# Kernel optimization log

Hardware: AMD Instinct MI355X
Metric: run time of the kernel (lower is better)

The kernel has to match this reference:

```python
import jax, jax.numpy as jnp
import numpy as np

N_ATOMS = 100_000
N_PAIRS = 3_200_000


def setup_inputs() -> dict:
    key = jax.random.key(0)
    k0, k1, k2, k3, k4 = jax.random.split(key, 5)
    atomic_numbers = jax.random.randint(k0, (N_ATOMS,), 1, 95, dtype=jnp.int32)
    distances = jax.random.uniform(k1, (N_PAIRS,), jnp.float32, 0.5, 5.0)
    cutoffs = jax.random.uniform(k2, (N_PAIRS,), jnp.float32)
    idx_i = jnp.sort(jax.random.randint(k3, (N_PAIRS,), 0, N_ATOMS, dtype=jnp.int32))
    idx_j = jax.random.randint(k4, (N_PAIRS,), 0, N_ATOMS, dtype=jnp.int32)
    # ZBL parameters (trainable=True defaults from __init__)
    a_coefficient = jnp.array([0.8854], dtype=jnp.float32)
    a_exponent = jnp.array([0.23], dtype=jnp.float32)
    phi_coefficients = jnp.array([0.18175, 0.50986, 0.28022, 0.02817], dtype=jnp.float32)
    phi_exponents = jnp.array([3.1998, 0.94229, 0.4029, 0.20162], dtype=jnp.float32)
    # unit conversion buffers: identity units -> factors = 1.0
    ke = jnp.array([1.0 / (4.0 * np.pi * 0.005526349406)], dtype=jnp.float32)
    distances_model2Ang = jnp.array([1.0], dtype=jnp.float32)
    energies_Hatree2model = jnp.array([1.0], dtype=jnp.float32)
    return dict(atomic_numbers=atomic_numbers, distances=distances, cutoffs=cutoffs,
                idx_i=idx_i, idx_j=idx_j, a_coefficient=a_coefficient,
                a_exponent=a_exponent, phi_coefficients=phi_coefficients,
                phi_exponents=phi_exponents, ke=ke,
                distances_model2Ang=distances_model2Ang,
                energies_Hatree2model=energies_Hatree2model)


def reference(atomic_numbers, distances, cutoffs, idx_i, idx_j,
              a_coefficient, a_exponent, phi_coefficients, phi_exponents,
              ke, distances_model2Ang, energies_Hatree2model):
    Z = atomic_numbers.astype(distances.dtype)            # [N]
    distances_ang = distances * distances_model2Ang        # [P]
    za = Z ** jnp.abs(a_exponent)                          # [N] (a_exponent is [1])
    a_ij = jnp.abs(a_coefficient) / (za[idx_i] + za[idx_j])  # [P]
    arguments = distances / a_ij                           # [P] (faithful: uses model-unit distances)
    # L1-normalized |phi_coefficients|
    abs_c = jnp.abs(phi_coefficients)
    coefficients = abs_c / jnp.sum(abs_c)                  # [4]
    exponents = jnp.abs(phi_exponents)                     # [4]
    # phi[p] = sum_k c_k * exp(-e_k * arg_p)  -> [P,4] intermediate
    phi = jnp.sum(coefficients[None, :] * jnp.exp(-exponents[None, :] * arguments[:, None]), axis=1)
    repulsion = ke * Z[idx_i] * Z[idx_j] / distances_ang * phi * cutoffs  # [P]
    Erep = energies_Hatree2model * jax.ops.segment_sum(repulsion, idx_i, num_segments=N_ATOMS)
    return Erep
```

## Files before the change

kernel.cpp:

```cpp
#include <hip/hip_runtime.h>
#include <math.h>

#define LOG2E 1.4426950408889634f

__global__ void __launch_bounds__(256)
zbl_prep(const int* __restrict__ Z, const float* __restrict__ a_exp,
         float2* __restrict__ zaz, float* __restrict__ out,
         int n_atoms, int out_n) {
    int i = blockIdx.x * blockDim.x + threadIdx.x;
    float aexp = fabsf(a_exp[0]);
    if (i < n_atoms) {
        float zf = (float)Z[i];
        float za = exp2f(aexp * __log2f(zf));
        zaz[i] = make_float2(za, zf);
    }
    if (i < out_n) out[i] = 0.0f;
}

__global__ void __launch_bounds__(256)
zbl_pairs8(const float* __restrict__ dist, const float* __restrict__ cut,
           const int* __restrict__ idx_i, const int* __restrict__ idx_j,
           const float2* __restrict__ zaz,
           const float* __restrict__ a_coef,
           const float* __restrict__ phi_c, const float* __restrict__ phi_e,
           const float* __restrict__ ke, const float* __restrict__ d2a,
           const float* __restrict__ e2m,
           float* __restrict__ out, int n) {
    float inv_ac = __fdividef(1.0f, fabsf(a_coef[0]));
    float c0 = fabsf(phi_c[0]), c1 = fabsf(phi_c[1]),
          c2 = fabsf(phi_c[2]), c3 = fabsf(phi_c[3]);
    float cnorm = __fdividef(1.0f, c0 + c1 + c2 + c3);
    c0 *= cnorm; c1 *= cnorm; c2 *= cnorm; c3 *= cnorm;
    float e0 = fabsf(phi_e[0]) * LOG2E, e1 = fabsf(phi_e[1]) * LOG2E,
          e2 = fabsf(phi_e[2]) * LOG2E, e3 = fabsf(phi_e[3]) * LOG2E;
    float scale = ke[0] * e2m[0] * __fdividef(1.0f, d2a[0]);

    int t   = threadIdx.x;
    int gid = blockIdx.x * blockDim.x + t;
    int p0  = gid * 8;

    int   k[8];
    float v[8];

    if (p0 + 7 < n) {
        const float4* dist4 = (const float4*)dist;
        const float4* cut4  = (const float4*)cut;
        const int4*   ii4   = (const int4*)idx_i;
        const int4*   jj4   = (const int4*)idx_j;
        float4 dA = dist4[2 * gid], dB = dist4[2 * gid + 1];
        float4 cA = cut4[2 * gid],  cB = cut4[2 * gid + 1];
        int4   iA = ii4[2 * gid],   iB = ii4[2 * gid + 1];
        int4   jA = jj4[2 * gid],   jB = jj4[2 * gid + 1];

        k[0] = iA.x; k[1] = iA.y; k[2] = iA.z; k[3] = iA.w;
        k[4] = iB.x; k[5] = iB.y; k[6] = iB.z; k[7] = iB.w;
        int j[8] = { jA.x, jA.y, jA.z, jA.w, jB.x, jB.y, jB.z, jB.w };
        float d[8] = { dA.x, dA.y, dA.z, dA.w, dB.x, dB.y, dB.z, dB.w };
        float cu[8] = { cA.x, cA.y, cA.z, cA.w, cB.x, cB.y, cB.z, cB.w };

        float2 gj[8];
        #pragma unroll
        for (int q = 0; q < 8; ++q) gj[q] = zaz[j[q]];

        float za_i[8], zf_i[8];
        {
            float2 g = zaz[k[0]];
            za_i[0] = g.x; zf_i[0] = g.y;
        }
        #pragma unroll
        for (int q = 1; q < 8; ++q) {
            if (k[q] != k[q - 1]) {
                float2 g = zaz[k[q]];
                za_i[q] = g.x; zf_i[q] = g.y;
            } else {
                za_i[q] = za_i[q - 1]; zf_i[q] = zf_i[q - 1];
            }
        }

        #pragma unroll
        for (int q = 0; q < 8; ++q) {
            float arg = d[q] * (za_i[q] + gj[q].x) * inv_ac;
            float phi = c0 * exp2f(-e0 * arg) + c1 * exp2f(-e1 * arg)
                      + c2 * exp2f(-e2 * arg) + c3 * exp2f(-e3 * arg);
            v[q] = scale * zf_i[q] * gj[q].y * phi * cu[q]
                 * __fdividef(1.0f, d[q]);
        }
    } else {
        #pragma unroll
        for (int q = 0; q < 8; ++q) {
            int p = p0 + q;
            if (p < n) {
                int ki = idx_i[p], jj = idx_j[p];
                float2 gi = zaz[ki], gjv = zaz[jj];
                float dd = dist[p];
                float arg = dd * (gi.x + gjv.x) * inv_ac;
                float phi = c0 * exp2f(-e0 * arg) + c1 * exp2f(-e1 * arg)
                          + c2 * exp2f(-e2 * arg) + c3 * exp2f(-e3 * arg);
                k[q] = ki;
                v[q] = scale * gi.y * gjv.y * phi * cut[p]
                     * __fdividef(1.0f, dd);
            } else {
                k[q] = (q > 0) ? k[q - 1] : -1;
                v[q] = 0.0f;
            }
        }
    }

    float run = v[0];
    float firstRun = 0.0f;
    bool  firstEnds = false;
    int   runStart = 0;
    #pragma unroll
    for (int q = 1; q < 8; ++q) {
        if (k[q] == k[q - 1]) {
            run += v[q];
        } else {
            if (runStart == 0) { firstRun = run; firstEnds = true; }
            else if (k[q - 1] >= 0) atomicAdd(out + k[q - 1], run);
            run = v[q];
            runStart = q;
        }
    }
    float c   = run;
    int   key = k[7];

    int lane = t & 63;
    #pragma unroll
    for (int off = 1; off < 64; off <<= 1) {
        float ov = __shfl_up(c, (unsigned)off, 64);
        int   ok = __shfl_up(key, (unsigned)off, 64);
        if (lane >= off && ok == key) c += ov;
    }

    float prev_c   = __shfl_up(c, 1u, 64);
    int   prev_key = __shfl_up(key, 1u, 64);
    int   next_k0  = __shfl_down(k[0], 1u, 64);

    if (k[0] >= 0 && firstEnds) {
        float tot = firstRun + ((lane > 0 && prev_key == k[0]) ? prev_c : 0.0f);
        atomicAdd(out + k[0], tot);
    }
    bool tail = (lane == 63) || (next_k0 != key);
    if (key >= 0 && tail) atomicAdd(out + key, c);
}

extern "C" void kernel_launch(void* const* d_in, const int* in_sizes, int n_in,
                              void* d_out, int out_size, void* d_ws, size_t ws_size,
                              hipStream_t stream) {
    const int*   atomic_numbers = (const int*)  d_in[0];
    const float* distances      = (const float*)d_in[1];
    const float* cutoffs        = (const float*)d_in[2];
    const int*   idx_i          = (const int*)  d_in[3];
    const int*   idx_j          = (const int*)  d_in[4];
    const float* a_coefficient  = (const float*)d_in[5];
    const float* a_exponent     = (const float*)d_in[6];
    const float* phi_coeffs     = (const float*)d_in[7];
    const float* phi_exps       = (const float*)d_in[8];
    const float* ke             = (const float*)d_in[9];
    const float* d2a            = (const float*)d_in[10];
    const float* e2m            = (const float*)d_in[11];
    float* out = (float*)d_out;

    const int n_atoms = in_sizes[0];
    const int n_pairs = in_sizes[1];

    const int block = 256;
    const int n_threads = (n_pairs + 7) / 8;
    const int grid_pairs = (n_threads + block - 1) / block;
    const int grid_prep  = (((n_atoms > out_size) ? n_atoms : out_size) + block - 1) / block;

    float2* zaz = (float2*)d_ws;
    zbl_prep<<<grid_prep, block, 0, stream>>>(
        atomic_numbers, a_exponent, zaz, out, n_atoms, out_size);
    zbl_pairs8<<<grid_pairs, block, 0, stream>>>(
        distances, cutoffs, idx_i, idx_j, zaz,
        a_coefficient, phi_coeffs, phi_exps, ke, d2a, e2m,
        out, n_pairs);
}
```

Measured before the change: 123.7 us.

## Compress per-atom table to uint8 Z with shared-memory Z^a lookup

```diff
diff --git a/kernel.cpp b/kernel.cpp
--- a/kernel.cpp
+++ b/kernel.cpp
@@ -4,28 +4,25 @@
 #define LOG2E 1.4426950408889634f
 
 __global__ void __launch_bounds__(256)
-zbl_prep(const int* __restrict__ Z, const float* __restrict__ a_exp,
-         float2* __restrict__ zaz, float* __restrict__ out,
-         int n_atoms, int out_n) {
+zbl_prep(const int* __restrict__ Z, unsigned char* __restrict__ z8,
+         float* __restrict__ out, int n_atoms, int out_n) {
     int i = blockIdx.x * blockDim.x + threadIdx.x;
-    float aexp = fabsf(a_exp[0]);
-    if (i < n_atoms) {
-        float zf = (float)Z[i];
-        float za = exp2f(aexp * __log2f(zf));
-        zaz[i] = make_float2(za, zf);
-    }
-    if (i < out_n) out[i] = 0.0f;
+    if (i < n_atoms) z8[i] = (unsigned char)Z[i];
+    if (i < out_n)   out[i] = 0.0f;
 }
 
 __global__ void __launch_bounds__(256)
 zbl_pairs8(const float* __restrict__ dist, const float* __restrict__ cut,
            const int* __restrict__ idx_i, const int* __restrict__ idx_j,
-           const float2* __restrict__ zaz,
-           const float* __restrict__ a_coef,
+           const unsigned char* __restrict__ z8,
+           const float* __restrict__ a_coef, const float* __restrict__ a_exp,
            const float* __restrict__ phi_c, const float* __restrict__ phi_e,
            const float* __restrict__ ke, const float* __restrict__ d2a,
            const float* __restrict__ e2m,
            float* __restrict__ out, int n) {
+    __shared__ float za_tab[128];
+
+    float aexp   = fabsf(a_exp[0]);
     float inv_ac = __fdividef(1.0f, fabsf(a_coef[0]));
     float c0 = fabsf(phi_c[0]), c1 = fabsf(phi_c[1]),
           c2 = fabsf(phi_c[2]), c3 = fabsf(phi_c[3]);
@@ -35,7 +32,10 @@
           e2 = fabsf(phi_e[2]) * LOG2E, e3 = fabsf(phi_e[3]) * LOG2E;
     float scale = ke[0] * e2m[0] * __fdividef(1.0f, d2a[0]);
 
-    int t   = threadIdx.x;
+    int t = threadIdx.x;
+    if (t < 128) za_tab[t] = (t >= 1) ? exp2f(aexp * __log2f((float)t)) : 0.0f;
+    __syncthreads();
+
     int gid = blockIdx.x * blockDim.x + t;
     int p0  = gid * 8;
 
@@ -55,34 +55,21 @@
         k[0] = iA.x; k[1] = iA.y; k[2] = iA.z; k[3] = iA.w;
         k[4] = iB.x; k[5] = iB.y; k[6] = iB.z; k[7] = iB.w;
         int j[8] = { jA.x, jA.y, jA.z, jA.w, jB.x, jB.y, jB.z, jB.w };
-        float d[8] = { dA.x, dA.y, dA.z, dA.w, dB.x, dB.y, dB.z, dB.w };
+        float d[8]  = { dA.x, dA.y, dA.z, dA.w, dB.x, dB.y, dB.z, dB.w };
         float cu[8] = { cA.x, cA.y, cA.z, cA.w, cB.x, cB.y, cB.z, cB.w };
 
-        float2 gj[8];
+        int zi[8], zj[8];
         #pragma unroll
-        for (int q = 0; q < 8; ++q) gj[q] = zaz[j[q]];
-
-        float za_i[8], zf_i[8];
-        {
-            float2 g = zaz[k[0]];
-            za_i[0] = g.x; zf_i[0] = g.y;
-        }
+        for (int q = 0; q < 8; ++q) zi[q] = (int)z8[k[q]];
         #pragma unroll
-        for (int q = 1; q < 8; ++q) {
-            if (k[q] != k[q - 1]) {
-                float2 g = zaz[k[q]];
-                za_i[q] = g.x; zf_i[q] = g.y;
-            } else {
-                za_i[q] = za_i[q - 1]; zf_i[q] = zf_i[q - 1];
-            }
-        }
+        for (int q = 0; q < 8; ++q) zj[q] = (int)z8[j[q]];
 
         #pragma unroll
         for (int q = 0; q < 8; ++q) {
-            float arg = d[q] * (za_i[q] + gj[q].x) * inv_ac;
+            float arg = d[q] * (za_tab[zi[q]] + za_tab[zj[q]]) * inv_ac;
             float phi = c0 * exp2f(-e0 * arg) + c1 * exp2f(-e1 * arg)
                       + c2 * exp2f(-e2 * arg) + c3 * exp2f(-e3 * arg);
-            v[q] = scale * zf_i[q] * gj[q].y * phi * cu[q]
+            v[q] = scale * (float)(zi[q] * zj[q]) * phi * cu[q]
                  * __fdividef(1.0f, d[q]);
         }
     } else {
@@ -91,13 +78,13 @@
             int p = p0 + q;
             if (p < n) {
                 int ki = idx_i[p], jj = idx_j[p];
-                float2 gi = zaz[ki], gjv = zaz[jj];
+                int zi = (int)z8[ki], zj = (int)z8[jj];
                 float dd = dist[p];
-                float arg = dd * (gi.x + gjv.x) * inv_ac;
+                float arg = dd * (za_tab[zi] + za_tab[zj]) * inv_ac;
                 float phi = c0 * exp2f(-e0 * arg) + c1 * exp2f(-e1 * arg)
                           + c2 * exp2f(-e2 * arg) + c3 * exp2f(-e3 * arg);
                 k[q] = ki;
-                v[q] = scale * gi.y * gjv.y * phi * cut[p]
+                v[q] = scale * (float)(zi * zj) * phi * cut[p]
                      * __fdividef(1.0f, dd);
             } else {
                 k[q] = (q > 0) ? k[q - 1] : -1;
@@ -169,11 +156,11 @@
     const int grid_pairs = (n_threads + block - 1) / block;
     const int grid_prep  = (((n_atoms > out_size) ? n_atoms : out_size) + block - 1) / block;
 
-    float2* zaz = (float2*)d_ws;
+    unsigned char* z8 = (unsigned char*)d_ws;
     zbl_prep<<<grid_prep, block, 0, stream>>>(
-        atomic_numbers, a_exponent, zaz, out, n_atoms, out_size);
+        atomic_numbers, z8, out, n_atoms, out_size);
     zbl_pairs8<<<grid_pairs, block, 0, stream>>>(
-        distances, cutoffs, idx_i, idx_j, zaz,
-        a_coefficient, phi_coeffs, phi_exps, ke, d2a, e2m,
+        distances, cutoffs, idx_i, idx_j, z8,
+        a_coefficient, a_exponent, phi_coeffs, phi_exps, ke, d2a, e2m,
         out, n_pairs);
 }
```

Result: faster. 117.4 us (-5.1%).
